# Optimization experiments

Hardware: AMD Instinct MI355X
Metric: run time of the kernel (lower is better)

The kernel has to match this reference:

```python
import jax, jax.numpy as jnp
import numpy as np

SCALE_FACTOR = 1.0
VIS_MAX = 1024


def setup_inputs() -> dict:
    key = jax.random.key(0)
    kq, kk, kv = jax.random.split(key, 3)
    B, C, H, W = 4, 256, 64, 64
    Q = jax.random.normal(kq, (B, C, H, W), dtype=jnp.float32)
    K = jax.random.normal(kk, (B, C, H, W), dtype=jnp.float32)
    V = jax.random.normal(kv, (B, C, H, W), dtype=jnp.float32)
    return {"Q": Q, "K": K, "V": V}


def reference(Q, K, V):
    # Q,K: [B,C,H,W] -> flatten spatial dims to HW
    B, C, H, W = Q.shape
    HW = H * W
    Q_flat = Q.reshape(B, C, HW).transpose(0, 2, 1)  # [B, HW, C]
    K_flat = K.reshape(B, C, HW)                      # [B, C, HW]
    # Full scaled score matrix [B, HW, HW]; argmax over keys reproduces the
    # chunked running-max/argmax (strict '>' update keeps first max, matching
    # jnp.argmax tie-breaking).
    S = jnp.einsum('bqc,bck->bqk', Q_flat, K_flat) * SCALE_FACTOR
    H_idx = jnp.argmax(S, axis=2).astype(jnp.int64)   # [B, HW]
    vis = min(VIS_MAX, HW)
    S_vis = S[:, :vis, :vis]                          # [B, vis, vis]
    return S_vis, H_idx
```

## Files before the change

### kernel.cpp

```cpp
#include <hip/hip_runtime.h>
#include <stdint.h>

#define B_   4
#define C_   256
#define HW_  4096
#define VIS_ 1024
#define KE_  768

using half8   = __attribute__((ext_vector_type(8))) _Float16;
using floatx4 = __attribute__((ext_vector_type(4))) float;

__device__ __forceinline__ unsigned mapf(float v) {
    unsigned u = __float_as_uint(v);
    return (u & 0x80000000u) ? ~u : (u | 0x80000000u);
}

__global__ void init_ws_kernel(unsigned long long* ws, int n) {
    int i = blockIdx.x * blockDim.x + threadIdx.x;
    if (i < n) ws[i] = 0ull;
}

__global__ void finalize_kernel(const unsigned long long* __restrict__ ws,
                                float* __restrict__ out1, int n) {
    int i = blockIdx.x * blockDim.x + threadIdx.x;
    if (i < n) {
        unsigned kinv = (unsigned)(ws[i] & 0xFFFFFFFFull);
        out1[i] = (float)(HW_ - 1 - (int)kinv);
    }
}


__global__ __launch_bounds__(256) void split_transpose_kernel(
    const float* __restrict__ Q, const float* __restrict__ K,
    _Float16* __restrict__ Aexp, _Float16* __restrict__ Bexp,
    unsigned long long* __restrict__ keys)
{
    __shared__ float tile[64][65];
    const int t = threadIdx.x;
    if (blockIdx.y == 0 && blockIdx.z == 0)
        keys[blockIdx.x * 256 + t] = 0ull;

    const int hw0 = blockIdx.x * 64;
    const int c0  = blockIdx.y * 64;
    const int z = blockIdx.z, b = z >> 1, which = z & 1;
    const float* src = (which ? K : Q) + (size_t)b * C_ * HW_;
    _Float16* dst = (which ? Bexp : Aexp) + (size_t)b * HW_ * KE_;

    #pragma unroll
    for (int i = 0; i < 4; ++i) {
        int c  = (t >> 4) + i * 16;
        int hw = (t & 15) * 4;
        float4 v = *(const float4*)(src + (size_t)(c0 + c) * HW_ + hw0 + hw);
        tile[c][hw] = v.x; tile[c][hw+1] = v.y; tile[c][hw+2] = v.z; tile[c][hw+3] = v.w;
    }
    __syncthreads();

    #pragma unroll
    for (int i = 0; i < 2; ++i) {
        int id  = t + i * 256;
        int row = id >> 3;
        int c8  = (id & 7) * 8;
        half8 h8, l8;
        #pragma unroll
        for (int j = 0; j < 8; ++j) {
            float v = tile[c8 + j][row];
            _Float16 h = (_Float16)v;
            h8[j] = h;
            l8[j] = (_Float16)(v - (float)h);
        }
        _Float16* base = dst + (size_t)(hw0 + row) * KE_ + c0 + c8;
        *(half8*)(base + 0 * C_) = h8;
        *(half8*)(base + 1 * C_) = which ? l8 : h8;
        *(half8*)(base + 2 * C_) = which ? h8 : l8;
    }
}

__device__ __forceinline__ void gl2lds16(const _Float16* g, _Float16* l) {
    __builtin_amdgcn_global_load_lds(
        (const __attribute__((address_space(1))) void*)g,
        (__attribute__((address_space(3))) void*)l, 16, 0, 0);
}


#define BARRIER __builtin_amdgcn_s_barrier()
#define LGKM0   asm volatile("s_waitcnt lgkmcnt(0)" ::: "memory")
#define VMC(n)  asm volatile("s_waitcnt vmcnt(" #n ")" ::: "memory")
#define SCHEDB  __builtin_amdgcn_sched_barrier(0)

__device__ __forceinline__ void stage_half(const _Float16* __restrict__ g,
                                           _Float16* lb, int t, int kbase)
{
    #pragma unroll
    for (int j = 0; j < 2; ++j) {
        const int c   = t + j * 512;
        const int row = c >> 2;
        const int ch  = (c & 3) ^ ((row >> 1) & 3);
        gl2lds16(g + (size_t)row * KE_ + kbase + ch * 8, lb + c * 8);
    }
}

template<int MQ>
__device__ __forceinline__ void ds_load_a(const _Float16* base, int wave_m, int s,
                                          int quad, half8 (&a)[4]) {
    #pragma unroll
    for (int mi = 0; mi < 4; ++mi) {
        int row = wave_m * 128 + MQ * 64 + mi * 16 + s;
        int ch  = quad ^ ((row >> 1) & 3);
        a[mi] = *(const half8*)(base + row * 32 + ch * 8);
    }
}

__device__ __forceinline__ void ds_load_b(const _Float16* base, int wave_n, int s,
                                          int quad, half8 (&bfr)[4]) {
    #pragma unroll
    for (int ni = 0; ni < 4; ++ni) {
        int col = wave_n * 64 + ni * 16 + s;
        int ch  = quad ^ ((col >> 1) & 3);
        bfr[ni] = *(const half8*)(base + col * 32 + ch * 8);
    }
}

template<int MQ>
__device__ __forceinline__ void do_mfma(const half8 (&a)[4], const half8 (&bfr)[4],
                                        floatx4 (&acc)[8][4]) {
    __builtin_amdgcn_s_setprio(1);
    #pragma unroll
    for (int mi = 0; mi < 4; ++mi)
        #pragma unroll
        for (int ni = 0; ni < 4; ++ni)
            acc[MQ * 4 + mi][ni] = __builtin_amdgcn_mfma_f32_16x16x32_f16(
                a[mi], bfr[ni], acc[MQ * 4 + mi][ni], 0, 0, 0);
    __builtin_amdgcn_s_setprio(0);
}

__global__ __launch_bounds__(512, 1) void gemm_mfma_kernel(
    const _Float16* __restrict__ Aexp, const _Float16* __restrict__ Bexp,
    float* __restrict__ out0, unsigned long long* __restrict__ keys)
{
    __shared__ __align__(16) _Float16 lds[65536];

    const int t      = threadIdx.x;
    const int lane   = t & 63;
    const int wave   = t >> 6;
    const int quad   = lane >> 4;
    const int s      = lane & 15;
    const int wave_m = wave >> 2;
    const int wave_n = wave & 3;

    const int n    = blockIdx.x;
    const int wgid = (n & 7) * 128 + (n >> 3);
    const int kt   = wgid & 15;
    const int qt   = (wgid >> 4) & 15;
    const int b    = wgid >> 8;

    const _Float16* Agl = Aexp + (size_t)b * HW_ * KE_ + (size_t)(qt * 256) * KE_;
    const _Float16* Bgl = Bexp + (size_t)b * HW_ * KE_ + (size_t)(kt * 256) * KE_;

    stage_half(Agl, lds + 0 * 8192, t, 0);
    stage_half(Bgl, lds + 1 * 8192, t, 0);
    stage_half(Agl, lds + 2 * 8192, t, 32);
    stage_half(Bgl, lds + 3 * 8192, t, 32);
    stage_half(Agl, lds + 4 * 8192, t, 64);
    stage_half(Bgl, lds + 5 * 8192, t, 64);
    VMC(8);
    BARRIER; SCHEDB;

    half8 a[4], bfr[4];
    floatx4 acc[8][4] = {};

    #pragma unroll 1
    for (int T = 0; T < 21; ++T) {
        const int db  = T & 3;
        const int db3 = (T + 3) & 3;
        const _Float16* Ar = lds + (db * 2 + 0) * 8192;
        const _Float16* Br = lds + (db * 2 + 1) * 8192;
        _Float16* As = lds + (db3 * 2 + 0) * 8192;
        _Float16* Bs = lds + (db3 * 2 + 1) * 8192;
        const int kb3 = (T + 3) * 32;

        ds_load_a<0>(Ar, wave_m, s, quad, a);
        ds_load_b(Br, wave_n, s, quad, bfr);
        stage_half(Agl, As, t, kb3);
        BARRIER; LGKM0;
        do_mfma<0>(a, bfr, acc);
        BARRIER;
        ds_load_a<1>(Ar, wave_m, s, quad, a);
        stage_half(Bgl, Bs, t, kb3);
        BARRIER; LGKM0;
        do_mfma<1>(a, bfr, acc);
        VMC(8);
        BARRIER; SCHEDB;
    }

    VMC(0);
    __syncthreads();

    #pragma unroll
    for (int T = 21; T < 24; ++T) {
        const _Float16* Ar = lds + ((T & 3) * 2 + 0) * 8192;
        const _Float16* Br = lds + ((T & 3) * 2 + 1) * 8192;
        ds_load_a<0>(Ar, wave_m, s, quad, a);
        ds_load_b(Br, wave_n, s, quad, bfr);
        do_mfma<0>(a, bfr, acc);
        ds_load_a<1>(Ar, wave_m, s, quad, a);
        do_mfma<1>(a, bfr, acc);
    }

    if (qt < 4 && kt < 4) {
        #pragma unroll
        for (int mi8 = 0; mi8 < 8; ++mi8)
            #pragma unroll
            for (int r = 0; r < 4; ++r) {
                int grow = qt * 256 + wave_m * 128 + mi8 * 16 + quad * 4 + r;
                float* orow = out0 + ((size_t)b * VIS_ + grow) * VIS_ + kt * 256 + wave_n * 64;
                #pragma unroll
                for (int ni = 0; ni < 4; ++ni)
                    orow[ni * 16 + s] = acc[mi8][ni][r];
            }
    }

    __syncthreads();
    unsigned long long* red = (unsigned long long*)lds;

    #pragma unroll
    for (int mi8 = 0; mi8 < 8; ++mi8) {
        #pragma unroll
        for (int r = 0; r < 4; ++r) {
            float best = acc[mi8][0][r];
            int bcol = wave_n * 64 + s;
            #pragma unroll
            for (int ni = 1; ni < 4; ++ni) {
                float v = acc[mi8][ni][r];
                if (v > best) { best = v; bcol = wave_n * 64 + ni * 16 + s; }
            }
            int gcol = kt * 256 + bcol;
            unsigned long long key = ((unsigned long long)mapf(best) << 32)
                                   | (unsigned)(HW_ - 1 - gcol);
            #pragma unroll
            for (int m = 1; m < 16; m <<= 1) {
                unsigned long long o = __shfl_xor(key, m, 64);
                if (o > key) key = o;
            }
            if (s == 0)
                red[(wave_m * 128 + mi8 * 16 + quad * 4 + r) * 4 + wave_n] = key;
        }
    }
    __syncthreads();
    if (t < 256) {
        const unsigned long long* rr = red + t * 4;
        unsigned long long k0 = rr[0], k1 = rr[1], k2 = rr[2], k3 = rr[3];
        unsigned long long m01 = k0 > k1 ? k0 : k1;
        unsigned long long m23 = k2 > k3 ? k2 : k3;
        atomicMax(&keys[(size_t)b * HW_ + qt * 256 + t], m01 > m23 ? m01 : m23);
    }
}

#define BT   64
#define BK   32
#define LDP  68

__global__ __launch_bounds__(256) void gemm_argmax_kernel(
    const float* __restrict__ Q, const float* __restrict__ K,
    float* __restrict__ out0, unsigned long long* __restrict__ ws)
{
    __shared__ float As[BK][LDP];
    __shared__ float Bs[BK][LDP];
    __shared__ unsigned long long red[BT][17];

    const int t  = threadIdx.x;
    const int tx = t & 15;
    const int ty = t >> 4;
    const int k0 = blockIdx.x * BT;
    const int q0 = blockIdx.y * BT;
    const int b  = blockIdx.z;

    const float* Qb = Q + (size_t)b * C_ * HW_;
    const float* Kb = K + (size_t)b * C_ * HW_;

    float acc[4][4] = {{0.f},{0.f},{0.f},{0.f}};

    for (int c0 = 0; c0 < C_; c0 += BK) {
        #pragma unroll
        for (int i = 0; i < 2; ++i) {
            int idx = i * 256 + t;
            int row = idx >> 4;
            int col = (idx & 15) * 4;
            const float4 a  = *(const float4*)(Qb + (size_t)(c0 + row) * HW_ + q0 + col);
            const float4 bv = *(const float4*)(Kb + (size_t)(c0 + row) * HW_ + k0 + col);
            *(float4*)(&As[row][col]) = a;
            *(float4*)(&Bs[row][col]) = bv;
        }
        __syncthreads();
        #pragma unroll
        for (int cc = 0; cc < BK; ++cc) {
            const float4 av = *(const float4*)(&As[cc][ty * 4]);
            const float4 bv = *(const float4*)(&Bs[cc][tx * 4]);
            const float a_[4] = {av.x, av.y, av.z, av.w};
            const float b_[4] = {bv.x, bv.y, bv.z, bv.w};
            #pragma unroll
            for (int i = 0; i < 4; ++i)
                #pragma unroll
                for (int j = 0; j < 4; ++j)
                    acc[i][j] = fmaf(a_[i], b_[j], acc[i][j]);
        }
        __syncthreads();
    }

    if (q0 < VIS_ && k0 < VIS_) {
        #pragma unroll
        for (int i = 0; i < 4; ++i) {
            float4 v = make_float4(acc[i][0], acc[i][1], acc[i][2], acc[i][3]);
            size_t off = (size_t)b * VIS_ * VIS_ + (size_t)(q0 + ty * 4 + i) * VIS_ + (k0 + tx * 4);
            *(float4*)(out0 + off) = v;
        }
    }

    #pragma unroll
    for (int i = 0; i < 4; ++i) {
        float best = acc[i][0];
        int   bj   = 0;
        #pragma unroll
        for (int j = 1; j < 4; ++j)
            if (acc[i][j] > best) { best = acc[i][j]; bj = j; }
        int kidx = k0 + tx * 4 + bj;
        unsigned long long key = ((unsigned long long)mapf(best) << 32)
                               | (unsigned)(HW_ - 1 - kidx);
        red[ty * 4 + i][tx] = key;
    }
    __syncthreads();
    if (t < BT) {
        unsigned long long best = red[t][0];
        #pragma unroll
        for (int j = 1; j < 16; ++j) {
            unsigned long long v = red[t][j];
            if (v > best) best = v;
        }
        atomicMax(&ws[(size_t)b * HW_ + q0 + t], best);
    }
}

extern "C" void kernel_launch(void* const* d_in, const int* in_sizes, int n_in,
                              void* d_out, int out_size, void* d_ws, size_t ws_size,
                              hipStream_t stream) {
    const float* Q = (const float*)d_in[0];
    const float* K = (const float*)d_in[1];
    float* out0 = (float*)d_out;
    float* out1 = out0 + (size_t)B_ * VIS_ * VIS_;

    unsigned long long* keys = (unsigned long long*)d_ws;
    const size_t keys_bytes = (size_t)B_ * HW_ * 8;
    const size_t exp_elems  = (size_t)B_ * HW_ * KE_;
    const size_t need = keys_bytes + 2 * exp_elems * sizeof(_Float16);

    const int n = B_ * HW_;

    if (ws_size >= need) {
        _Float16* Aexp = (_Float16*)((char*)d_ws + keys_bytes);
        _Float16* Bexp = Aexp + exp_elems;
        split_transpose_kernel<<<dim3(HW_ / 64, C_ / 64, 2 * B_), 256, 0, stream>>>(Q, K, Aexp, Bexp, keys);
        gemm_mfma_kernel<<<dim3((HW_ / 256) * (HW_ / 256) * B_), 512, 0, stream>>>(Aexp, Bexp, out0, keys);
    } else {
        init_ws_kernel<<<(n + 255) / 256, 256, 0, stream>>>(keys, n);
        gemm_argmax_kernel<<<dim3(HW_ / BT, HW_ / BT, B_), 256, 0, stream>>>(Q, K, out0, keys);
    }

    finalize_kernel<<<(n + 255) / 256, 256, 0, stream>>>(keys, out1, n);
}
```

Baseline: 214.9 us.

## Software-pipeline LDS fragment loads against MFMA with register double-buffering

Restructures the GEMM main loop so LDS reads for the next half-tile (split A halves and B fragment pairs) are issued before the MFMAs on the current fragments, using separate aM0/aM1 and bA/bB register sets. It prefetches four K stages instead of three and rewrites the epilogue to drain them. The launch bound changes to ask for 2 blocks per CU. The aim is to hide LDS latency behind matrix math. In exchange it raises register pressure, and the 2-block bound could force spills given the large accumulator array. The 64K-half LDS buffer (128 KB) may also block a second resident block.

```diff
diff --git a/kernel.cpp b/kernel.cpp
--- a/kernel.cpp
+++ b/kernel.cpp
@@ -110,10 +110,11 @@
     }
 }
 
-__device__ __forceinline__ void ds_load_b(const _Float16* base, int wave_n, int s,
-                                          int quad, half8 (&bfr)[4]) {
-    #pragma unroll
-    for (int ni = 0; ni < 4; ++ni) {
+template<int NI0>
+__device__ __forceinline__ void ds_load_b2(const _Float16* base, int wave_n, int s,
+                                           int quad, half8 (&bfr)[4]) {
+    #pragma unroll
+    for (int ni = NI0; ni < NI0 + 2; ++ni) {
         int col = wave_n * 64 + ni * 16 + s;
         int ch  = quad ^ ((col >> 1) & 3);
         bfr[ni] = *(const half8*)(base + col * 32 + ch * 8);
@@ -133,7 +134,7 @@
     __builtin_amdgcn_s_setprio(0);
 }
 
-__global__ __launch_bounds__(512, 1) void gemm_mfma_kernel(
+__global__ __launch_bounds__(512, 2) void gemm_mfma_kernel(
     const _Float16* __restrict__ Aexp, const _Float16* __restrict__ Bexp,
     float* __restrict__ out0, unsigned long long* __restrict__ keys)
 {
@@ -156,55 +157,95 @@
     const _Float16* Agl = Aexp + (size_t)b * HW_ * KE_ + (size_t)(qt * 256) * KE_;
     const _Float16* Bgl = Bexp + (size_t)b * HW_ * KE_ + (size_t)(kt * 256) * KE_;
 
-    stage_half(Agl, lds + 0 * 8192, t, 0);
-    stage_half(Bgl, lds + 1 * 8192, t, 0);
-    stage_half(Agl, lds + 2 * 8192, t, 32);
-    stage_half(Bgl, lds + 3 * 8192, t, 32);
-    stage_half(Agl, lds + 4 * 8192, t, 64);
-    stage_half(Bgl, lds + 5 * 8192, t, 64);
+    #define AR(db) (lds + (db) * 2 * 8192)
+    #define BR(db) (lds + ((db) * 2 + 1) * 8192)
+
+    stage_half(Agl, AR(0), t, 0);
+    stage_half(Bgl, BR(0), t, 0);
+    stage_half(Agl, AR(1), t, 32);
+    stage_half(Bgl, BR(1), t, 32);
+    stage_half(Agl, AR(2), t, 64);
+    stage_half(Bgl, BR(2), t, 64);
+    stage_half(Agl, AR(3), t, 96);
+    stage_half(Bgl, BR(3), t, 96);
     VMC(8);
     BARRIER; SCHEDB;
 
-    half8 a[4], bfr[4];
+    half8 aM0[4], aM1[4], bA[4], bB[4];
     floatx4 acc[8][4] = {};
 
+    ds_load_a<0>(AR(0), wave_m, s, quad, aM0);
+    ds_load_b2<0>(BR(0), wave_n, s, quad, bA);
+    ds_load_b2<2>(BR(0), wave_n, s, quad, bA);
+    LGKM0;
+    BARRIER; SCHEDB;
+
     #pragma unroll 1
-    for (int T = 0; T < 21; ++T) {
-        const int db  = T & 3;
-        const int db3 = (T + 3) & 3;
-        const _Float16* Ar = lds + (db * 2 + 0) * 8192;
-        const _Float16* Br = lds + (db * 2 + 1) * 8192;
-        _Float16* As = lds + (db3 * 2 + 0) * 8192;
-        _Float16* Bs = lds + (db3 * 2 + 1) * 8192;
-        const int kb3 = (T + 3) * 32;
-
-        ds_load_a<0>(Ar, wave_m, s, quad, a);
-        ds_load_b(Br, wave_n, s, quad, bfr);
-        stage_half(Agl, As, t, kb3);
-        BARRIER; LGKM0;
-        do_mfma<0>(a, bfr, acc);
-        BARRIER;
-        ds_load_a<1>(Ar, wave_m, s, quad, a);
-        stage_half(Bgl, Bs, t, kb3);
-        BARRIER; LGKM0;
-        do_mfma<1>(a, bfr, acc);
+    for (int j = 0; j < 10; ++j) {
+        const int T0  = 2 * j;
+        const int db0 = T0 & 3, db1 = (T0 + 1) & 3, db2 = (T0 + 2) & 3;
+        ds_load_a<1>(AR(db0), wave_m, s, quad, aM1);
+        ds_load_b2<0>(BR(db1), wave_n, s, quad, bB);
+        do_mfma<0>(aM0, bA, acc);
+        LGKM0;
+        BARRIER; SCHEDB;
+        stage_half(Agl, AR(db0), t, (T0 + 4) * 32);
+        stage_half(Bgl, BR(db0), t, (T0 + 4) * 32);
+        ds_load_b2<2>(BR(db1), wave_n, s, quad, bB);
+        ds_load_a<0>(AR(db1), wave_m, s, quad, aM0);
+        do_mfma<1>(aM1, bA, acc);
+        LGKM0;
         VMC(8);
         BARRIER; SCHEDB;
-    }
-
+        ds_load_a<1>(AR(db1), wave_m, s, quad, aM1);
+        ds_load_b2<0>(BR(db2), wave_n, s, quad, bA);
+        do_mfma<0>(aM0, bB, acc);
+        LGKM0;
+        BARRIER; SCHEDB;
+        stage_half(Agl, AR(db1), t, (T0 + 5) * 32);
+        stage_half(Bgl, BR(db1), t, (T0 + 5) * 32);
+        ds_load_b2<2>(BR(db2), wave_n, s, quad, bA);
+        ds_load_a<0>(AR(db2), wave_m, s, quad, aM0);
+        do_mfma<1>(aM1, bB, acc);
+        LGKM0;
+        VMC(8);
+        BARRIER; SCHEDB;
+    }
+
+    ds_load_a<1>(AR(0), wave_m, s, quad, aM1);
+    ds_load_b2<0>(BR(1), wave_n, s, quad, bB);
+    do_mfma<0>(aM0, bA, acc);
+    LGKM0;
+    BARRIER; SCHEDB;
+    ds_load_b2<2>(BR(1), wave_n, s, quad, bB);
+    ds_load_a<0>(AR(1), wave_m, s, quad, aM0);
+    do_mfma<1>(aM1, bA, acc);
+    LGKM0;
+    VMC(4);
+    BARRIER; SCHEDB;
+    ds_load_a<1>(AR(1), wave_m, s, quad, aM1);
+    ds_load_b2<0>(BR(2), wave_n, s, quad, bA);
+    do_mfma<0>(aM0, bB, acc);
+    LGKM0;
+    BARRIER; SCHEDB;
+    ds_load_b2<2>(BR(2), wave_n, s, quad, bA);
+    ds_load_a<0>(AR(2), wave_m, s, quad, aM0);
+    do_mfma<1>(aM1, bB, acc);
+    LGKM0;
     VMC(0);
-    __syncthreads();
-
-    #pragma unroll
-    for (int T = 21; T < 24; ++T) {
-        const _Float16* Ar = lds + ((T & 3) * 2 + 0) * 8192;
-        const _Float16* Br = lds + ((T & 3) * 2 + 1) * 8192;
-        ds_load_a<0>(Ar, wave_m, s, quad, a);
-        ds_load_b(Br, wave_n, s, quad, bfr);
-        do_mfma<0>(a, bfr, acc);
-        ds_load_a<1>(Ar, wave_m, s, quad, a);
-        do_mfma<1>(a, bfr, acc);
-    }
+    BARRIER; SCHEDB;
+    ds_load_a<1>(AR(2), wave_m, s, quad, aM1);
+    do_mfma<0>(aM0, bA, acc);
+    do_mfma<1>(aM1, bA, acc);
+    ds_load_a<0>(AR(3), wave_m, s, quad, aM0);
+    ds_load_a<1>(AR(3), wave_m, s, quad, aM1);
+    ds_load_b2<0>(BR(3), wave_n, s, quad, bB);
+    ds_load_b2<2>(BR(3), wave_n, s, quad, bB);
+    do_mfma<0>(aM0, bB, acc);
+    do_mfma<1>(aM1, bB, acc);
+
+    #undef AR
+    #undef BR
 
     if (qt < 4 && kt < 4) {
         #pragma unroll
```

Result: no change. 218.1 us (+1.5%).

## Store hi/lo fp16 split once and reuse A/B fragments across split products

Applied to the files above, without the earlier changes.

The split-fp16 operands used to be stored as a 768-wide expanded K dimension that duplicated the hi parts. They are now stored as 512-wide hi|lo, and the GEMM stages hi and lo chunks side by side. Each chunk does Ah*Bh, Ah*Bl and Al*Bh, reusing fragments already in registers. This cuts the global bytes written by the transpose and read by the GEMM, along with LDS traffic per MFMA. In exchange the pipeline is restructured into a 2-stage double buffer with coarser chunks, and launch_bounds is changed to (512,2), which may pressure registers given the 128 KB of LDS.

```diff
diff --git a/kernel.cpp b/kernel.cpp
--- a/kernel.cpp
+++ b/kernel.cpp
@@ -5,7 +5,7 @@
 #define C_   256
 #define HW_  4096
 #define VIS_ 1024
-#define KE_  768
+#define KE2  512
 
 using half8   = __attribute__((ext_vector_type(8))) _Float16;
 using floatx4 = __attribute__((ext_vector_type(4))) float;
@@ -44,7 +44,7 @@
     const int c0  = blockIdx.y * 64;
     const int z = blockIdx.z, b = z >> 1, which = z & 1;
     const float* src = (which ? K : Q) + (size_t)b * C_ * HW_;
-    _Float16* dst = (which ? Bexp : Aexp) + (size_t)b * HW_ * KE_;
+    _Float16* dst = (which ? Bexp : Aexp) + (size_t)b * HW_ * KE2;
 
     #pragma unroll
     for (int i = 0; i < 4; ++i) {
@@ -68,10 +68,9 @@
             h8[j] = h;
             l8[j] = (_Float16)(v - (float)h);
         }
-        _Float16* base = dst + (size_t)(hw0 + row) * KE_ + c0 + c8;
+        _Float16* base = dst + (size_t)(hw0 + row) * KE2 + c0 + c8;
         *(half8*)(base + 0 * C_) = h8;
-        *(half8*)(base + 1 * C_) = which ? l8 : h8;
-        *(half8*)(base + 2 * C_) = which ? h8 : l8;
+        *(half8*)(base + 1 * C_) = l8;
     }
 }
 
@@ -95,8 +94,18 @@
         const int c   = t + j * 512;
         const int row = c >> 2;
         const int ch  = (c & 3) ^ ((row >> 1) & 3);
-        gl2lds16(g + (size_t)row * KE_ + kbase + ch * 8, lb + c * 8);
-    }
+        gl2lds16(g + (size_t)row * KE2 + kbase + ch * 8, lb + c * 8);
+    }
+}
+
+__device__ __forceinline__ void stage_chunk(const _Float16* __restrict__ Agl,
+                                            const _Float16* __restrict__ Bgl,
+                                            _Float16* lds, int p, int c, int t)
+{
+    stage_half(Agl, lds + (p * 4 + 0) * 8192, t, c * 32);
+    stage_half(Agl, lds + (p * 4 + 1) * 8192, t, 256 + c * 32);
+    stage_half(Bgl, lds + (p * 4 + 2) * 8192, t, c * 32);
+    stage_half(Bgl, lds + (p * 4 + 3) * 8192, t, 256 + c * 32);
 }
 
 template<int MQ>
@@ -133,7 +142,29 @@
     __builtin_amdgcn_s_setprio(0);
 }
 
-__global__ __launch_bounds__(512, 1) void gemm_mfma_kernel(
+__device__ __forceinline__ void chunk_compute(const _Float16* lds, int p,
+    int wave_m, int wave_n, int s, int quad, floatx4 (&acc)[8][4])
+{
+    const _Float16* Ah = lds + (p * 4 + 0) * 8192;
+    const _Float16* Al = lds + (p * 4 + 1) * 8192;
+    const _Float16* Bh = lds + (p * 4 + 2) * 8192;
+    const _Float16* Bl = lds + (p * 4 + 3) * 8192;
+    half8 a0[4], a1[4], bh[4], bl[4];
+    ds_load_a<0>(Ah, wave_m, s, quad, a0);
+    ds_load_a<1>(Ah, wave_m, s, quad, a1);
+    ds_load_b(Bh, wave_n, s, quad, bh);
+    do_mfma<0>(a0, bh, acc);
+    do_mfma<1>(a1, bh, acc);
+    ds_load_b(Bl, wave_n, s, quad, bl);
+    do_mfma<0>(a0, bl, acc);
+    do_mfma<1>(a1, bl, acc);
+    ds_load_a<0>(Al, wave_m, s, quad, a0);
+    ds_load_a<1>(Al, wave_m, s, quad, a1);
+    do_mfma<0>(a0, bh, acc);
+    do_mfma<1>(a1, bh, acc);
+}
+
+__global__ __launch_bounds__(512, 2) void gemm_mfma_kernel(
     const _Float16* __restrict__ Aexp, const _Float16* __restrict__ Bexp,
     float* __restrict__ out0, unsigned long long* __restrict__ keys)
 {
@@ -153,58 +184,31 @@
     const int qt   = (wgid >> 4) & 15;
     const int b    = wgid >> 8;
 
-    const _Float16* Agl = Aexp + (size_t)b * HW_ * KE_ + (size_t)(qt * 256) * KE_;
-    const _Float16* Bgl = Bexp + (size_t)b * HW_ * KE_ + (size_t)(kt * 256) * KE_;
-
-    stage_half(Agl, lds + 0 * 8192, t, 0);
-    stage_half(Bgl, lds + 1 * 8192, t, 0);
-    stage_half(Agl, lds + 2 * 8192, t, 32);
-    stage_half(Bgl, lds + 3 * 8192, t, 32);
-    stage_half(Agl, lds + 4 * 8192, t, 64);
-    stage_half(Bgl, lds + 5 * 8192, t, 64);
+    const _Float16* Agl = Aexp + (size_t)b * HW_ * KE2 + (size_t)(qt * 256) * KE2;
+    const _Float16* Bgl = Bexp + (size_t)b * HW_ * KE2 + (size_t)(kt * 256) * KE2;
+
+    stage_chunk(Agl, Bgl, lds, 0, 0, t);
+    stage_chunk(Agl, Bgl, lds, 1, 1, t);
     VMC(8);
     BARRIER; SCHEDB;
 
-    half8 a[4], bfr[4];
     floatx4 acc[8][4] = {};
 
     #pragma unroll 1
-    for (int T = 0; T < 21; ++T) {
-        const int db  = T & 3;
-        const int db3 = (T + 3) & 3;
-        const _Float16* Ar = lds + (db * 2 + 0) * 8192;
-        const _Float16* Br = lds + (db * 2 + 1) * 8192;
-        _Float16* As = lds + (db3 * 2 + 0) * 8192;
-        _Float16* Bs = lds + (db3 * 2 + 1) * 8192;
-        const int kb3 = (T + 3) * 32;
-
-        ds_load_a<0>(Ar, wave_m, s, quad, a);
-        ds_load_b(Br, wave_n, s, quad, bfr);
-        stage_half(Agl, As, t, kb3);
-        BARRIER; LGKM0;
-        do_mfma<0>(a, bfr, acc);
+    for (int c = 0; c < 6; ++c) {
+        chunk_compute(lds, c & 1, wave_m, wave_n, s, quad, acc);
+        LGKM0;
         BARRIER;
-        ds_load_a<1>(Ar, wave_m, s, quad, a);
-        stage_half(Bgl, Bs, t, kb3);
-        BARRIER; LGKM0;
-        do_mfma<1>(a, bfr, acc);
+        stage_chunk(Agl, Bgl, lds, c & 1, c + 2, t);
         VMC(8);
         BARRIER; SCHEDB;
     }
-
+    chunk_compute(lds, 0, wave_m, wave_n, s, quad, acc);
+    LGKM0;
+    BARRIER;
     VMC(0);
-    __syncthreads();
-
-    #pragma unroll
-    for (int T = 21; T < 24; ++T) {
-        const _Float16* Ar = lds + ((T & 3) * 2 + 0) * 8192;
-        const _Float16* Br = lds + ((T & 3) * 2 + 1) * 8192;
-        ds_load_a<0>(Ar, wave_m, s, quad, a);
-        ds_load_b(Br, wave_n, s, quad, bfr);
-        do_mfma<0>(a, bfr, acc);
-        ds_load_a<1>(Ar, wave_m, s, quad, a);
-        do_mfma<1>(a, bfr, acc);
-    }
+    BARRIER; SCHEDB;
+    chunk_compute(lds, 1, wave_m, wave_n, s, quad, acc);
 
     if (qt < 4 && kt < 4) {
         #pragma unroll
@@ -349,7 +353,7 @@
 
     unsigned long long* keys = (unsigned long long*)d_ws;
     const size_t keys_bytes = (size_t)B_ * HW_ * 8;
-    const size_t exp_elems  = (size_t)B_ * HW_ * KE_;
+    const size_t exp_elems  = (size_t)B_ * HW_ * KE2;
     const size_t need = keys_bytes + 2 * exp_elems * sizeof(_Float16);
 
     const int n = B_ * HW_;
```

Result: faster. 208.1 us (-3.2%).
